# Kernel optimization log

Measured on AMD Instinct MI355X. Metric: run time of the kernel, lower is better.

## Reference

```python
import jax, jax.numpy as jnp
import numpy as np

EPS = 1e-08
K_N = 10
K_E = 10
F_DIM = 512
SCALE = F_DIM ** -0.5
N_NODES = 16384
N_EDGES = 2048


def layernorm(x, w, b):
    mu = x.mean(axis=-1, keepdims=True)
    var = x.var(axis=-1, keepdims=True)
    return (x - mu) * jax.lax.rsqrt(var + 1e-5) * w + b


def mask_attn(attn, k):
    # topk along last dim, scatter boolean mask, elementwise masking
    _, idx = jax.lax.top_k(attn, k)
    rows = jnp.arange(attn.shape[0])[:, None]
    mask = jnp.zeros(attn.shape, dtype=bool).at[rows, idx].set(True)
    return attn * mask


def setup_inputs() -> dict:
    key = jax.random.key(0)
    ks = jax.random.split(key, 12)
    d, h = F_DIM, 512  # hidden = max(f_dim, 128)
    w = 0.02  # weight init scale to keep softmax unsaturated
    return {
        'inputs': jax.random.normal(ks[0], (N_NODES, d), jnp.float32),
        'noise': jax.random.normal(ks[1], (N_EDGES, d), jnp.float32),
        'edges_mu': jax.random.normal(ks[2], (1, d), jnp.float32),
        'edges_logsigma': jnp.zeros((1, d), jnp.float32),
        'Wq': jax.random.normal(ks[3], (d, d), jnp.float32) * w,
        'bq': jnp.zeros((d,), jnp.float32),
        'Wk': jax.random.normal(ks[4], (d, d), jnp.float32) * w,
        'bk': jnp.zeros((d,), jnp.float32),
        'Wv': jax.random.normal(ks[5], (d, d), jnp.float32) * w,
        'bv': jnp.zeros((d,), jnp.float32),
        'W1': jax.random.normal(ks[6], (2 * d, h), jnp.float32) * w,
        'b1': jnp.zeros((h,), jnp.float32),
        'W2': jax.random.normal(ks[7], (h, d), jnp.float32) * w,
        'b2': jnp.zeros((d,), jnp.float32),
        'ln_in_w': jnp.ones((d,), jnp.float32),
        'ln_in_b': jnp.zeros((d,), jnp.float32),
        'ln_e_w': jnp.ones((d,), jnp.float32),
        'ln_e_b': jnp.zeros((d,), jnp.float32),
    }


def reference(inputs, noise, edges_mu, edges_logsigma, Wq, bq, Wk, bk, Wv, bv,
              W1, b1, W2, b2, ln_in_w, ln_in_b, ln_e_w, ln_e_b):
    relu = jax.nn.relu
    # slot init: mu + sigma * noise  -> [n_s, d]
    edges = edges_mu + jnp.exp(edges_logsigma) * noise
    x = layernorm(inputs, ln_in_w, ln_in_b)          # [n, d]
    k = relu(x @ Wk + bk)                            # [n, d]
    v = relu(x @ Wv + bv)                            # [n, d]
    # single iteration (iters=1)
    e = layernorm(edges, ln_e_w, ln_e_b)             # [n_s, d]
    q = relu(e @ Wq + bq)                            # [n_s, d]
    dots = (q @ k.T) * SCALE                         # [n_s, n]
    attn = jax.nn.softmax(dots, axis=1) + EPS
    attn = attn / attn.sum(axis=1, keepdims=True)
    attn = mask_attn(attn, K_N)
    updates = attn @ v                               # [n_s, d]
    e = jnp.concatenate([e, updates], axis=1)        # [n_s, 2d]
    e = relu(e @ W1 + b1) @ W2 + b2                  # mlp -> [n_s, d]
    q2 = x @ Wq + bq                                 # note: no activation here
    k2 = relu(e @ Wk + bk)                           # [n_s, d]
    dots2 = (q2 @ k2.T) * SCALE                      # [n, n_s]
    attn_v = jax.nn.softmax(dots2, axis=1)
    H = mask_attn(attn_v, K_E)
    return e, H, dots2
```

## Files before the change

kernel.cpp:

```cpp
#include <hip/hip_runtime.h>
#include <stdint.h>


#define NN 16384
#define NE 2048
#define TOPK 10

static const float SCALE_F = 0.04419417382415922f;
#define EPS_F 1e-8f

using bf16x8  = __attribute__((ext_vector_type(8))) __bf16;
using floatx4 = __attribute__((ext_vector_type(4))) float;

__device__ __forceinline__ unsigned f_as_u(float f) {
  union { float f; unsigned u; } v; v.f = f; return v.u;
}
__device__ __forceinline__ float u_as_f(unsigned u) {
  union { unsigned u; float f; } v; v.u = u; return v.f;
}
__device__ __forceinline__ unsigned short f2bf(float f) {
  unsigned u = f_as_u(f);
  unsigned r = u + 0x7fffu + ((u >> 16) & 1u);
  return (unsigned short)(r >> 16);
}
__device__ __forceinline__ float bf2f(unsigned short h) {
  return u_as_f(((unsigned)h) << 16);
}

__device__ __forceinline__ void glds16(const unsigned short* g, unsigned short* l) {
  __builtin_amdgcn_global_load_lds(
      (const __attribute__((address_space(1))) unsigned int*)g,
      (__attribute__((address_space(3))) unsigned int*)l, 16, 0, 0);
}

__device__ __forceinline__ unsigned fkey(float f) {
  unsigned u = f_as_u(f);
  return (u & 0x80000000u) ? ~u : (u | 0x80000000u);
}
__device__ __forceinline__ float funkey(unsigned k) {
  unsigned u = (k & 0x80000000u) ? (k ^ 0x80000000u) : ~k;
  return u_as_f(u);
}
__device__ __forceinline__ unsigned long long packkc(float v, int col) {
  return ((unsigned long long)fkey(v) << 32) | (unsigned)(~(unsigned)col);
}
__device__ __forceinline__ int unpack_col(unsigned long long w) {
  return (int)(~(unsigned)(w & 0xFFFFFFFFull));
}
__device__ __forceinline__ float unpack_val(unsigned long long w) {
  return funkey((unsigned)(w >> 32));
}
__device__ __forceinline__ unsigned long long shfl_xor_u64(unsigned long long x, int m) {
  unsigned lo = (unsigned)x, hi = (unsigned)(x >> 32);
  lo = __shfl_xor(lo, m, 64);
  hi = __shfl_xor(hi, m, 64);
  return ((unsigned long long)hi << 32) | lo;
}

__global__ void transpose_cast_kernel(const float* __restrict__ src,
                                      unsigned short* __restrict__ dhi,
                                      unsigned short* __restrict__ dlo,
                                      int K, int N) {
  __shared__ float tile[32][33];
  int n0 = blockIdx.x * 32, k0 = blockIdx.y * 32;
  int tx = threadIdx.x, ty = threadIdx.y;
  for (int r = ty; r < 32; r += 8)
    tile[r][tx] = src[(size_t)(k0 + r) * N + n0 + tx];
  __syncthreads();
  for (int r = ty; r < 32; r += 8) {
    float v = tile[tx][r];
    size_t o = (size_t)(n0 + r) * K + k0 + tx;
    unsigned short h = f2bf(v);
    dhi[o] = h;
    if (dlo) dlo[o] = f2bf(v - bf2f(h));
  }
}

__global__ void transpose_cast3_kernel(const float* __restrict__ s0,
                                       const float* __restrict__ s1,
                                       const float* __restrict__ s2,
                                       unsigned short* __restrict__ dhi) {
  __shared__ float tile[32][33];
  const float* src = blockIdx.z == 0 ? s0 : (blockIdx.z == 1 ? s1 : s2);
  unsigned short* d = dhi + (size_t)blockIdx.z * 512 * 512;
  int n0 = blockIdx.x * 32, k0 = blockIdx.y * 32;
  int tx = threadIdx.x, ty = threadIdx.y;
  for (int r = ty; r < 32; r += 8)
    tile[r][tx] = src[(size_t)(k0 + r) * 512 + n0 + tx];
  __syncthreads();
  for (int r = ty; r < 32; r += 8)
    d[(size_t)(n0 + r) * 512 + k0 + tx] = f2bf(tile[tx][r]);
}

__device__ __forceinline__ float block_sum_256(float v, float* sm4) {
#pragma unroll
  for (int off = 32; off; off >>= 1) v += __shfl_down(v, off, 64);
  __syncthreads();
  if ((threadIdx.x & 63) == 0) sm4[threadIdx.x >> 6] = v;
  __syncthreads();
  return (sm4[0] + sm4[1]) + (sm4[2] + sm4[3]);
}

__global__ __launch_bounds__(256) void ln_x_kernel(
    const float* __restrict__ in, const float* __restrict__ w,
    const float* __restrict__ b, unsigned short* __restrict__ out_hi) {
  __shared__ float sm4[4];
  int row = blockIdx.x, tid = threadIdx.x;
  const float* r = in + (size_t)row * 512;
  float x0 = r[tid], x1 = r[tid + 256];
  float mu = block_sum_256(x0 + x1, sm4) * (1.0f / 512.0f);
  float d0 = x0 - mu, d1 = x1 - mu;
  float var = block_sum_256(d0 * d0 + d1 * d1, sm4) * (1.0f / 512.0f);
  float rs = rsqrtf(var + 1e-5f);
  out_hi[(size_t)row * 512 + tid]       = f2bf(d0 * rs * w[tid] + b[tid]);
  out_hi[(size_t)row * 512 + tid + 256] = f2bf(d1 * rs * w[tid + 256] + b[tid + 256]);
}

__global__ __launch_bounds__(256) void ln_e_kernel(
    const float* __restrict__ noise, const float* __restrict__ mu_e,
    const float* __restrict__ ls_e, const float* __restrict__ w,
    const float* __restrict__ b, unsigned short* __restrict__ e1_hi,
    unsigned short* __restrict__ e1_lo) {
  __shared__ float sm4[4];
  int row = blockIdx.x, tid = threadIdx.x;
  const float* r = noise + (size_t)row * 512;
  float x0 = mu_e[tid] + expf(ls_e[tid]) * r[tid];
  float x1 = mu_e[tid + 256] + expf(ls_e[tid + 256]) * r[tid + 256];
  float mu = block_sum_256(x0 + x1, sm4) * (1.0f / 512.0f);
  float d0 = x0 - mu, d1 = x1 - mu;
  float var = block_sum_256(d0 * d0 + d1 * d1, sm4) * (1.0f / 512.0f);
  float rs = rsqrtf(var + 1e-5f);
  float y0 = d0 * rs * w[tid] + b[tid];
  float y1 = d1 * rs * w[tid + 256] + b[tid + 256];
  size_t o = (size_t)row * 1024;
  unsigned short h0 = f2bf(y0), h1 = f2bf(y1);
  e1_hi[o + tid] = h0;             e1_lo[o + tid] = f2bf(y0 - bf2f(h0));
  e1_hi[o + tid + 256] = h1;       e1_lo[o + tid + 256] = f2bf(y1 - bf2f(h1));
}

#define GEMM128_CORE(A_, B_, bm_, bn_, acc_, SMEM_)                            \
  unsigned short* As = (unsigned short*)(SMEM_);                               \
  unsigned short* Bs = (unsigned short*)(SMEM_) + 4096;                        \
  {                                                                            \
    const unsigned short* gA0 = (A_) + ((bm_) + (tid >> 2)) * 512 + ((tid & 3) << 3); \
    const unsigned short* gA1 = gA0 + 64 * 512;                                \
    const unsigned short* gB0 = (B_) + ((bn_) + (tid >> 2)) * 512 + ((tid & 3) << 3); \
    const unsigned short* gB1 = gB0 + 64 * 512;                                \
    unsigned short* dA0 = &As[wave * 512];                                     \
    unsigned short* dA1 = &As[2048 + wave * 512];                              \
    unsigned short* dB0 = &Bs[wave * 512];                                     \
    unsigned short* dB1 = &Bs[2048 + wave * 512];                              \
    for (int k0 = 0; k0 < 512; k0 += 32) {                                     \
      glds16(gA0 + k0, dA0);                                                   \
      glds16(gA1 + k0, dA1);                                                   \
      glds16(gB0 + k0, dB0);                                                   \
      glds16(gB1 + k0, dB1);                                                   \
      __syncthreads();                                                         \
      bf16x8 af0 = *(const bf16x8*)&As[(wave * 32 + lrow) * 32 + quad * 8];    \
      bf16x8 af1 = *(const bf16x8*)&As[(wave * 32 + 16 + lrow) * 32 + quad * 8]; \
      _Pragma("unroll")                                                        \
      for (int t = 0; t < 8; ++t) {                                            \
        bf16x8 bfr = *(const bf16x8*)&Bs[(t * 16 + lrow) * 32 + quad * 8];     \
        acc_[0][t] = __builtin_amdgcn_mfma_f32_16x16x32_bf16(af0, bfr, acc_[0][t], 0, 0, 0); \
        acc_[1][t] = __builtin_amdgcn_mfma_f32_16x16x32_bf16(af1, bfr, acc_[1][t], 0, 0, 0); \
      }                                                                        \
      __syncthreads();                                                         \
    }                                                                          \
  }

#define XCD_PANEL_MAP(mt_, nt_, owns_m_)                                       \
  int bid = (int)blockIdx.x, xcd = bid & 7, idx = bid >> 3;                    \
  int per = ((owns_m_) ? (mt_) : (nt_)) >> 3;                                  \
  int pa = idx % per, pb = idx / per;                                          \
  size_t bm = (size_t)((owns_m_) ? (xcd * per + pa) : pb) * 128;               \
  size_t bn = (size_t)((owns_m_) ? pb : (xcd * per + pa)) * 128;

__global__ __launch_bounds__(256) void gemm128_dots_kernel(
    const unsigned short* __restrict__ A, const unsigned short* __restrict__ B,
    float alpha, float* __restrict__ C, int ldc, int mt, int nt, int owns_m) {
  __shared__ __align__(16) char smem[33792];
  int tid = threadIdx.x, wave = tid >> 6, lane = tid & 63;
  int lrow = lane & 15, quad = lane >> 4;
  XCD_PANEL_MAP(mt, nt, owns_m)
  floatx4 zero4 = {0.f, 0.f, 0.f, 0.f};
  floatx4 acc[2][8];
#pragma unroll
  for (int i = 0; i < 2; ++i)
#pragma unroll
    for (int t = 0; t < 8; ++t) acc[i][t] = zero4;
  GEMM128_CORE(A, B, bm, bn, acc, smem)
  __syncthreads();
  float* wb = (float*)smem + wave * (16 * 132);
#pragma unroll
  for (int i = 0; i < 2; ++i) {
#pragma unroll
    for (int t = 0; t < 8; ++t)
#pragma unroll
      for (int r = 0; r < 4; ++r)
        wb[(quad * 4 + r) * 132 + t * 16 + lrow] = acc[i][t][r] * alpha;
    __syncthreads();
    size_t rowbase = bm + wave * 32 + i * 16;
#pragma unroll
    for (int p = 0; p < 8; ++p) {
      int rr = p * 2 + (lane >> 5);
      float4 v = *(const float4*)&wb[rr * 132 + ((lane & 31) << 2)];
      *(float4*)&C[(rowbase + rr) * (size_t)ldc + bn + ((lane & 31) << 2)] = v;
    }
    __syncthreads();
  }
}

__global__ __launch_bounds__(256) void gemm128_kvq_kernel(
    const unsigned short* __restrict__ A, const unsigned short* __restrict__ B,
    const float* __restrict__ bk, const float* __restrict__ bv,
    const float* __restrict__ bq,
    unsigned short* __restrict__ khi, unsigned short* __restrict__ vhi,
    unsigned short* __restrict__ q2hi) {
  __shared__ __align__(16) char smem[17408];
  int tid = threadIdx.x, wave = tid >> 6, lane = tid & 63;
  int lrow = lane & 15, quad = lane >> 4;
  XCD_PANEL_MAP(128, 12, 1)
  floatx4 zero4 = {0.f, 0.f, 0.f, 0.f};
  floatx4 acc[2][8];
#pragma unroll
  for (int i = 0; i < 2; ++i)
#pragma unroll
    for (int t = 0; t < 8; ++t) acc[i][t] = zero4;
  GEMM128_CORE(A, B, bm, bn, acc, smem)
  int mat = (int)(bn >> 9);
  int colbase = (int)(bn & 511);
  const float* bias = mat == 0 ? bk : (mat == 1 ? bv : bq);
  unsigned short* dst = mat == 0 ? khi : (mat == 1 ? vhi : q2hi);
  bool relu = mat < 2;
  __syncthreads();
  unsigned short* wb = (unsigned short*)smem + wave * (16 * 136);
#pragma unroll
  for (int i = 0; i < 2; ++i) {
#pragma unroll
    for (int t = 0; t < 8; ++t) {
      float bvv = bias[colbase + t * 16 + lrow];
#pragma unroll
      for (int r = 0; r < 4; ++r) {
        float v = acc[i][t][r] + bvv;
        if (relu) v = fmaxf(v, 0.0f);
        wb[(quad * 4 + r) * 136 + t * 16 + lrow] = f2bf(v);
      }
    }
    __syncthreads();
    size_t rowbase = bm + wave * 32 + i * 16;
#pragma unroll
    for (int p = 0; p < 4; ++p) {
      int rr = p * 4 + (lane >> 4);
      uint4 v = *(const uint4*)&wb[rr * 136 + ((lane & 15) << 3)];
      *(uint4*)&dst[(rowbase + rr) * 512 + colbase + ((lane & 15) << 3)] = v;
    }
    __syncthreads();
  }
}

template <bool SPLIT, bool RELU, bool HAS_BIAS, bool WF32, bool WHI, bool WLO>
__global__ __launch_bounds__(256) void gemm64_kernel(
    const unsigned short* __restrict__ Ahi, const unsigned short* __restrict__ Alo, int lda,
    const unsigned short* __restrict__ Bhi, const unsigned short* __restrict__ Blo, int K,
    const float* __restrict__ bias, float alpha,
    float* __restrict__ Cf, int ldc,
    unsigned short* __restrict__ Chi, unsigned short* __restrict__ Clo, int ldcb) {
  __shared__ __align__(16) unsigned short AsH[64 * 32];
  __shared__ __align__(16) unsigned short BsH[64 * 32];
  __shared__ __align__(16) unsigned short AsL[64 * 32];
  __shared__ __align__(16) unsigned short BsL[64 * 32];
  int tid = threadIdx.x, wave = tid >> 6, lane = tid & 63;
  int lrow = lane & 15, quad = lane >> 4;
  size_t bm = (size_t)blockIdx.x * 64, bn = (size_t)blockIdx.y * 64;
  int row = tid >> 2, off = (tid & 3) << 3;
  size_t aoff = (bm + row) * (size_t)lda + off;
  size_t boff = (bn + row) * (size_t)K + off;

  floatx4 zero4 = {0.f, 0.f, 0.f, 0.f};
  floatx4 acc[4];
#pragma unroll
  for (int t = 0; t < 4; ++t) acc[t] = zero4;

  for (int k0 = 0; k0 < K; k0 += 32) {
    uint4 ah = *(const uint4*)(Ahi + aoff + k0);
    uint4 bh = *(const uint4*)(Bhi + boff + k0);
    uint4 al, bl;
    if (SPLIT) {
      al = *(const uint4*)(Alo + aoff + k0);
      bl = *(const uint4*)(Blo + boff + k0);
    }
    __syncthreads();
    *(uint4*)&AsH[tid * 8] = ah;
    *(uint4*)&BsH[tid * 8] = bh;
    if (SPLIT) {
      *(uint4*)&AsL[tid * 8] = al;
      *(uint4*)&BsL[tid * 8] = bl;
    }
    __syncthreads();
    int ai = (wave * 16 + lrow) * 32 + quad * 8;
    bf16x8 aH = *(const bf16x8*)&AsH[ai];
    bf16x8 aL;
    if (SPLIT) aL = *(const bf16x8*)&AsL[ai];
#pragma unroll
    for (int t = 0; t < 4; ++t) {
      int bi = (t * 16 + lrow) * 32 + quad * 8;
      bf16x8 bH = *(const bf16x8*)&BsH[bi];
      acc[t] = __builtin_amdgcn_mfma_f32_16x16x32_bf16(aH, bH, acc[t], 0, 0, 0);
      if (SPLIT) {
        bf16x8 bL = *(const bf16x8*)&BsL[bi];
        acc[t] = __builtin_amdgcn_mfma_f32_16x16x32_bf16(aH, bL, acc[t], 0, 0, 0);
        acc[t] = __builtin_amdgcn_mfma_f32_16x16x32_bf16(aL, bH, acc[t], 0, 0, 0);
      }
    }
  }
  size_t row0 = bm + wave * 16 + quad * 4;
#pragma unroll
  for (int t = 0; t < 4; ++t) {
    int col = (int)bn + t * 16 + lrow;
    float bv = HAS_BIAS ? bias[col] : 0.0f;
#pragma unroll
    for (int r = 0; r < 4; ++r) {
      float v = acc[t][r] * alpha + bv;
      if (RELU) v = fmaxf(v, 0.0f);
      if (WF32) Cf[(row0 + r) * (size_t)ldc + col] = v;
      if (WHI) {
        unsigned short h = f2bf(v);
        Chi[(row0 + r) * (size_t)ldcb + col] = h;
        if (WLO) Clo[(row0 + r) * (size_t)ldcb + col] = f2bf(v - bf2f(h));
      }
    }
  }
}

#define INSERT4(lv, li, v, col)                                   \
  do {                                                            \
    if ((v) > lv[3]) {                                            \
      float cv_ = (v); int ci_ = (col);                           \
      _Pragma("unroll")                                           \
      for (int j_ = 0; j_ < 4; ++j_) {                            \
        bool sw_ = (cv_ > lv[j_]);                                \
        float tv_ = sw_ ? lv[j_] : cv_;                           \
        int ti_ = sw_ ? li[j_] : ci_;                              \
        lv[j_] = sw_ ? cv_ : lv[j_];                              \
        li[j_] = sw_ ? ci_ : li[j_];                              \
        cv_ = tv_; ci_ = ti_;                                     \
      }                                                           \
    }                                                             \
  } while (0)

__global__ __launch_bounds__(256) void attn1_kernel(
    const float* __restrict__ dots,
    const unsigned short* __restrict__ vhi,
    unsigned short* __restrict__ e1_hi, unsigned short* __restrict__ e1_lo) {
  __shared__ float sm_m[4], sm_s[4];
  __shared__ unsigned long long wbest[4];
  __shared__ unsigned long long wkey_s[TOPK];

  int tid = threadIdx.x, wave = tid >> 6, lane = tid & 63;
  int rowi = blockIdx.x;
  const float4* r4 = (const float4*)(dots + (size_t)rowi * NN);

  float lv[4]; int li[4];
#pragma unroll
  for (int j = 0; j < 4; ++j) { lv[j] = -INFINITY; li[j] = 0x7fffffff; }
  unsigned long long selmask = 0ull;
  int taken = 0;

  float m_loc = -INFINITY, s_loc = 0.0f;
  for (int i = 0; i < 16; ++i) {
    float4 q = r4[tid + (i << 8)];
#pragma unroll
    for (int c = 0; c < 4; ++c) {
      float v = (&q.x)[c];
      int col = ((tid + (i << 8)) << 2) + c;
      if (v > m_loc) {
        s_loc = s_loc * __expf(m_loc - v) + 1.0f;
        m_loc = v;
      } else {
        s_loc += __expf(v - m_loc);
      }
      INSERT4(lv, li, v, col);
    }
  }
#pragma unroll
  for (int sft = 32; sft; sft >>= 1) {
    float om = __shfl_xor(m_loc, sft, 64);
    float os = __shfl_xor(s_loc, sft, 64);
    float M = fmaxf(m_loc, om);
    s_loc = s_loc * __expf(m_loc - M) + os * __expf(om - M);
    m_loc = M;
  }
  if (lane == 0) { sm_m[wave] = m_loc; sm_s[wave] = s_loc; }
  __syncthreads();
  float M = fmaxf(fmaxf(sm_m[0], sm_m[1]), fmaxf(sm_m[2], sm_m[3]));
  float Z = sm_s[0] * __expf(sm_m[0] - M) + sm_s[1] * __expf(sm_m[1] - M) +
            sm_s[2] * __expf(sm_m[2] - M) + sm_s[3] * __expf(sm_m[3] - M);

  for (int rnd = 0; rnd < TOPK; ++rnd) {
    unsigned long long key;
    if (taken < 4) {
      key = packkc(lv[0], li[0]);
    } else {
      key = 0ull;
      for (int i = 0; i < 16; ++i) {
        float4 q = r4[tid + (i << 8)];
#pragma unroll
        for (int c = 0; c < 4; ++c) {
          int sl = i * 4 + c;
          if (!((selmask >> sl) & 1ull)) {
            int col = ((tid + (i << 8)) << 2) + c;
            unsigned long long kk = packkc((&q.x)[c], col);
            if (kk > key) key = kk;
          }
        }
      }
    }
#pragma unroll
    for (int sft = 32; sft; sft >>= 1) {
      unsigned long long ok = shfl_xor_u64(key, sft);
      if (ok > key) key = ok;
    }
    if (lane == 0) wbest[wave] = key;
    __syncthreads();
    unsigned long long w = wbest[0];
    if (wbest[1] > w) w = wbest[1];
    if (wbest[2] > w) w = wbest[2];
    if (wbest[3] > w) w = wbest[3];
    if (tid == 0) wkey_s[rnd] = w;
    int wcol = unpack_col(w);
    if (((wcol >> 2) & 255) == tid) {
      int sl = ((wcol >> 10) << 2) | (wcol & 3);
      selmask |= (1ull << sl);
      if (taken < 4) {
#pragma unroll
        for (int j = 0; j < 3; ++j) { lv[j] = lv[j + 1]; li[j] = li[j + 1]; }
      }
      ++taken;
    }
    __syncthreads();
  }

  const float inv_den = 1.0f / (1.0f + (float)NN * EPS_F);
  float invZ = 1.0f / Z;
  float u0 = 0.f, u1 = 0.f;
#pragma unroll
  for (int j = 0; j < TOPK; ++j) {
    unsigned long long w = wkey_s[j];
    int col = unpack_col(w);
    float val = unpack_val(w);
    float a = (__expf(val - M) * invZ + EPS_F) * inv_den;
    const unsigned short* vr = vhi + (size_t)col * 512;
    u0 += a * bf2f(vr[tid]);
    u1 += a * bf2f(vr[tid + 256]);
  }
  size_t o = (size_t)rowi * 1024 + 512;
  unsigned short h0 = f2bf(u0), h1 = f2bf(u1);
  e1_hi[o + tid] = h0;             e1_lo[o + tid] = f2bf(u0 - bf2f(h0));
  e1_hi[o + tid + 256] = h1;       e1_lo[o + tid + 256] = f2bf(u1 - bf2f(h1));
}

__global__ __launch_bounds__(256) void attn2_kernel(const float* __restrict__ dots2,
                                                    float* __restrict__ Hout) {
  int tid = threadIdx.x, wave = tid >> 6, lane = tid & 63;
  int rowi = blockIdx.x * 4 + wave;
  const float4* r4 = (const float4*)(dots2 + (size_t)rowi * NE);

  float d[32];
  float m = -INFINITY;
#pragma unroll
  for (int i = 0; i < 8; ++i) {
    float4 q = r4[lane + (i << 6)];
#pragma unroll
    for (int c = 0; c < 4; ++c) {
      d[i * 4 + c] = (&q.x)[c];
      m = fmaxf(m, d[i * 4 + c]);
    }
  }
#pragma unroll
  for (int sft = 32; sft; sft >>= 1) m = fmaxf(m, __shfl_xor(m, sft, 64));

  float s = 0.f;
#pragma unroll
  for (int j = 0; j < 32; ++j) { d[j] = __expf(d[j] - m); s += d[j]; }
#pragma unroll
  for (int sft = 32; sft; sft >>= 1) s += __shfl_xor(s, sft, 64);
  float invZ = 1.0f / s;

  float lv[4]; int li[4];
#pragma unroll
  for (int j = 0; j < 4; ++j) { lv[j] = -INFINITY; li[j] = 0x7fffffff; }
#pragma unroll
  for (int i = 0; i < 8; ++i) {
#pragma unroll
    for (int c = 0; c < 4; ++c) {
      int col = ((lane + (i << 6)) << 2) + c;
      INSERT4(lv, li, d[i * 4 + c], col);
    }
  }

  unsigned selmask = 0;
  int taken = 0;
  for (int rnd = 0; rnd < TOPK; ++rnd) {
    unsigned long long key;
    if (taken < 4) {
      key = packkc(lv[0], li[0]);
    } else {
      key = 0ull;
#pragma unroll
      for (int j = 0; j < 32; ++j) {
        if (!((selmask >> j) & 1u)) {
          int col = ((lane + ((j >> 2) << 6)) << 2) + (j & 3);
          unsigned long long kk = packkc(d[j], col);
          if (kk > key) key = kk;
        }
      }
    }
#pragma unroll
    for (int sft = 32; sft; sft >>= 1) {
      unsigned long long ok = shfl_xor_u64(key, sft);
      if (ok > key) key = ok;
    }
    int wcol = unpack_col(key);
    if (((wcol >> 2) & 63) == lane) {
      int sl = ((wcol >> 8) << 2) | (wcol & 3);
      selmask |= (1u << sl);
      if (taken < 4) {
#pragma unroll
        for (int j = 0; j < 3; ++j) { lv[j] = lv[j + 1]; li[j] = li[j + 1]; }
      }
      ++taken;
    }
  }

  float* hr = Hout + (size_t)rowi * NE;
#pragma unroll
  for (int i = 0; i < 8; ++i) {
    float4 o;
#pragma unroll
    for (int c = 0; c < 4; ++c) {
      int sl = i * 4 + c;
      (&o.x)[c] = ((selmask >> sl) & 1u) ? d[sl] * invZ : 0.0f;
    }
    ((float4*)hr)[lane + (i << 6)] = o;
  }
}

extern "C" void kernel_launch(void* const* d_in, const int* in_sizes, int n_in,
                              void* d_out, int out_size, void* d_ws, size_t ws_size,
                              hipStream_t stream) {
  (void)in_sizes; (void)n_in; (void)out_size; (void)ws_size;
  const float* inputs  = (const float*)d_in[0];
  const float* noise   = (const float*)d_in[1];
  const float* edges_mu = (const float*)d_in[2];
  const float* edges_ls = (const float*)d_in[3];
  const float* Wq = (const float*)d_in[4];
  const float* bq = (const float*)d_in[5];
  const float* Wk = (const float*)d_in[6];
  const float* bk = (const float*)d_in[7];
  const float* Wv = (const float*)d_in[8];
  const float* bv = (const float*)d_in[9];
  const float* W1 = (const float*)d_in[10];
  const float* b1 = (const float*)d_in[11];
  const float* W2 = (const float*)d_in[12];
  const float* b2 = (const float*)d_in[13];
  const float* ln_in_w = (const float*)d_in[14];
  const float* ln_in_b = (const float*)d_in[15];
  const float* ln_e_w = (const float*)d_in[16];
  const float* ln_e_b = (const float*)d_in[17];

  float* out_e  = (float*)d_out;
  float* out_H  = out_e + (size_t)NE * 512;
  float* out_d2 = out_H + (size_t)NN * NE;

  const size_t MB = 1024 * 1024;
  unsigned char* hb = (unsigned char*)out_H;
  unsigned short* x_hi  = (unsigned short*)(hb);
  unsigned short* k_hi  = (unsigned short*)(hb + 16 * MB);
  unsigned short* v_hi  = (unsigned short*)(hb + 32 * MB);
  unsigned short* q2_hi = (unsigned short*)(hb + 48 * MB);
  unsigned short* WcatT = (unsigned short*)(hb + 64 * MB);
  unsigned short* W1Th  = (unsigned short*)(hb + 66 * MB);
  unsigned short* W1Tl  = (unsigned short*)(hb + 67 * MB);
  unsigned short* W2Th  = (unsigned short*)(hb + 68 * MB);
  unsigned short* W2Tl  = (unsigned short*)(hb + 68 * MB + 512 * 1024);
  unsigned short* e1_hi = (unsigned short*)(hb + 70 * MB);
  unsigned short* e1_lo = (unsigned short*)(hb + 74 * MB);
  unsigned short* q_hi  = (unsigned short*)(hb + 78 * MB);
  unsigned short* h_hi  = (unsigned short*)(hb + 80 * MB);
  unsigned short* h_lo  = (unsigned short*)(hb + 82 * MB);
  unsigned short* e_hi  = (unsigned short*)(hb + 84 * MB);
  unsigned short* WkT   = WcatT;
  unsigned short* WqT   = WcatT + (size_t)1024 * 512;
  float* dots = out_d2;
  unsigned short* k2_hi = (unsigned short*)d_ws;

  dim3 tb(256);
  dim3 t32(32, 8);

  transpose_cast3_kernel<<<dim3(16, 16, 3), t32, 0, stream>>>(Wk, Wv, Wq, WcatT);
  transpose_cast_kernel<<<dim3(16, 32), t32, 0, stream>>>(W1, W1Th, W1Tl, 1024, 512);
  transpose_cast_kernel<<<dim3(16, 16), t32, 0, stream>>>(W2, W2Th, W2Tl, 512, 512);

  ln_x_kernel<<<NN, tb, 0, stream>>>(inputs, ln_in_w, ln_in_b, x_hi);
  ln_e_kernel<<<NE, tb, 0, stream>>>(noise, edges_mu, edges_ls, ln_e_w, ln_e_b, e1_hi, e1_lo);

  gemm128_kvq_kernel<<<dim3(1536), tb, 0, stream>>>(
      x_hi, WcatT, bk, bv, bq, k_hi, v_hi, q2_hi);
  gemm64_kernel<false, true, true, false, true, false><<<dim3(32, 8), tb, 0, stream>>>(
      e1_hi, nullptr, 1024, WqT, nullptr, 512, bq, 1.f, nullptr, 0, q_hi, nullptr, 512);
  gemm128_dots_kernel<<<dim3(2048), tb, 0, stream>>>(
      q_hi, k_hi, SCALE_F, dots, NN, 16, 128, 0);
  attn1_kernel<<<NE, tb, 0, stream>>>(dots, v_hi, e1_hi, e1_lo);
  gemm64_kernel<true, true, true, false, true, true><<<dim3(32, 8), tb, 0, stream>>>(
      e1_hi, e1_lo, 1024, W1Th, W1Tl, 1024, b1, 1.f, nullptr, 0, h_hi, h_lo, 512);
  gemm64_kernel<true, false, true, true, true, false><<<dim3(32, 8), tb, 0, stream>>>(
      h_hi, h_lo, 512, W2Th, W2Tl, 512, b2, 1.f, out_e, 512, e_hi, nullptr, 512);
  gemm64_kernel<false, true, true, false, true, false><<<dim3(32, 8), tb, 0, stream>>>(
      e_hi, nullptr, 512, WkT, nullptr, 512, bk, 1.f, nullptr, 0, k2_hi, nullptr, 512);
  gemm128_dots_kernel<<<dim3(2048), tb, 0, stream>>>(
      q2_hi, k2_hi, SCALE_F, out_d2, NE, 128, 16, 1);
  attn2_kernel<<<NN / 4, tb, 0, stream>>>(out_d2, out_H);
}
```

Baseline: 571.3 us.

## Merge prep kernels, fold q GEMM into kvq, widen GEMM K-tile with swizzled LDS

Three weight-transpose launches become one kernel, and the two layernorm launches become one, which cuts launch count. The separate q projection GEMM is folded into the kvq GEMM launch as 64 extra blocks. The 128x128 GEMM core now loads a 64-wide K slice per iteration into an XOR-swizzled shared-memory layout, halving the number of barrier pairs and aiming to reduce LDS bank conflicts. The gemm64 kernel also register-prefetches the next K slice, at the cost of larger shared-memory use and more registers.

```diff
diff --git a/kernel.cpp b/kernel.cpp
--- a/kernel.cpp
+++ b/kernel.cpp
@@ -57,15 +57,33 @@
   return ((unsigned long long)hi << 32) | lo;
 }
 
-__global__ void transpose_cast_kernel(const float* __restrict__ src,
-                                      unsigned short* __restrict__ dhi,
-                                      unsigned short* __restrict__ dlo,
-                                      int K, int N) {
+__global__ void transpose_all_kernel(
+    const float* __restrict__ Wk, const float* __restrict__ Wv,
+    const float* __restrict__ Wq, unsigned short* __restrict__ WcatT,
+    const float* __restrict__ W1, unsigned short* __restrict__ W1Th,
+    unsigned short* __restrict__ W1Tl,
+    const float* __restrict__ W2, unsigned short* __restrict__ W2Th,
+    unsigned short* __restrict__ W2Tl) {
   __shared__ float tile[32][33];
+  int z = blockIdx.z;
+  if (z != 3 && blockIdx.y >= 16) return;
+  const float* src;
+  unsigned short* dhi;
+  unsigned short* dlo;
+  int K;
+  if (z < 3) {
+    src = z == 0 ? Wk : (z == 1 ? Wv : Wq);
+    dhi = WcatT + (size_t)z * 512 * 512;
+    dlo = nullptr; K = 512;
+  } else if (z == 3) {
+    src = W1; dhi = W1Th; dlo = W1Tl; K = 1024;
+  } else {
+    src = W2; dhi = W2Th; dlo = W2Tl; K = 512;
+  }
   int n0 = blockIdx.x * 32, k0 = blockIdx.y * 32;
   int tx = threadIdx.x, ty = threadIdx.y;
   for (int r = ty; r < 32; r += 8)
-    tile[r][tx] = src[(size_t)(k0 + r) * N + n0 + tx];
+    tile[r][tx] = src[(size_t)(k0 + r) * 512 + n0 + tx];
   __syncthreads();
   for (int r = ty; r < 32; r += 8) {
     float v = tile[tx][r];
@@ -76,22 +94,6 @@
   }
 }
 
-__global__ void transpose_cast3_kernel(const float* __restrict__ s0,
-                                       const float* __restrict__ s1,
-                                       const float* __restrict__ s2,
-                                       unsigned short* __restrict__ dhi) {
-  __shared__ float tile[32][33];
-  const float* src = blockIdx.z == 0 ? s0 : (blockIdx.z == 1 ? s1 : s2);
-  unsigned short* d = dhi + (size_t)blockIdx.z * 512 * 512;
-  int n0 = blockIdx.x * 32, k0 = blockIdx.y * 32;
-  int tx = threadIdx.x, ty = threadIdx.y;
-  for (int r = ty; r < 32; r += 8)
-    tile[r][tx] = src[(size_t)(k0 + r) * 512 + n0 + tx];
-  __syncthreads();
-  for (int r = ty; r < 32; r += 8)
-    d[(size_t)(n0 + r) * 512 + k0 + tx] = f2bf(tile[tx][r]);
-}
-
 __device__ __forceinline__ float block_sum_256(float v, float* sm4) {
 #pragma unroll
   for (int off = 32; off; off >>= 1) v += __shfl_down(v, off, 64);
@@ -101,79 +103,90 @@
   return (sm4[0] + sm4[1]) + (sm4[2] + sm4[3]);
 }
 
-__global__ __launch_bounds__(256) void ln_x_kernel(
+__global__ __launch_bounds__(256) void ln_all_kernel(
     const float* __restrict__ in, const float* __restrict__ w,
-    const float* __restrict__ b, unsigned short* __restrict__ out_hi) {
-  __shared__ float sm4[4];
-  int row = blockIdx.x, tid = threadIdx.x;
-  const float* r = in + (size_t)row * 512;
-  float x0 = r[tid], x1 = r[tid + 256];
-  float mu = block_sum_256(x0 + x1, sm4) * (1.0f / 512.0f);
-  float d0 = x0 - mu, d1 = x1 - mu;
-  float var = block_sum_256(d0 * d0 + d1 * d1, sm4) * (1.0f / 512.0f);
-  float rs = rsqrtf(var + 1e-5f);
-  out_hi[(size_t)row * 512 + tid]       = f2bf(d0 * rs * w[tid] + b[tid]);
-  out_hi[(size_t)row * 512 + tid + 256] = f2bf(d1 * rs * w[tid + 256] + b[tid + 256]);
-}
-
-__global__ __launch_bounds__(256) void ln_e_kernel(
+    const float* __restrict__ b, unsigned short* __restrict__ out_hi,
     const float* __restrict__ noise, const float* __restrict__ mu_e,
-    const float* __restrict__ ls_e, const float* __restrict__ w,
-    const float* __restrict__ b, unsigned short* __restrict__ e1_hi,
+    const float* __restrict__ ls_e, const float* __restrict__ we,
+    const float* __restrict__ be, unsigned short* __restrict__ e1_hi,
     unsigned short* __restrict__ e1_lo) {
   __shared__ float sm4[4];
   int row = blockIdx.x, tid = threadIdx.x;
-  const float* r = noise + (size_t)row * 512;
-  float x0 = mu_e[tid] + expf(ls_e[tid]) * r[tid];
-  float x1 = mu_e[tid + 256] + expf(ls_e[tid + 256]) * r[tid + 256];
-  float mu = block_sum_256(x0 + x1, sm4) * (1.0f / 512.0f);
-  float d0 = x0 - mu, d1 = x1 - mu;
-  float var = block_sum_256(d0 * d0 + d1 * d1, sm4) * (1.0f / 512.0f);
-  float rs = rsqrtf(var + 1e-5f);
-  float y0 = d0 * rs * w[tid] + b[tid];
-  float y1 = d1 * rs * w[tid + 256] + b[tid + 256];
-  size_t o = (size_t)row * 1024;
-  unsigned short h0 = f2bf(y0), h1 = f2bf(y1);
-  e1_hi[o + tid] = h0;             e1_lo[o + tid] = f2bf(y0 - bf2f(h0));
-  e1_hi[o + tid + 256] = h1;       e1_lo[o + tid + 256] = f2bf(y1 - bf2f(h1));
-}
-
-#define GEMM128_CORE(A_, B_, bm_, bn_, acc_, SMEM_)                            \
+  if (row < NN) {
+    const float* r = in + (size_t)row * 512;
+    float x0 = r[tid], x1 = r[tid + 256];
+    float mu = block_sum_256(x0 + x1, sm4) * (1.0f / 512.0f);
+    float d0 = x0 - mu, d1 = x1 - mu;
+    float var = block_sum_256(d0 * d0 + d1 * d1, sm4) * (1.0f / 512.0f);
+    float rs = rsqrtf(var + 1e-5f);
+    out_hi[(size_t)row * 512 + tid]       = f2bf(d0 * rs * w[tid] + b[tid]);
+    out_hi[(size_t)row * 512 + tid + 256] = f2bf(d1 * rs * w[tid + 256] + b[tid + 256]);
+  } else {
+    row -= NN;
+    const float* r = noise + (size_t)row * 512;
+    float x0 = mu_e[tid] + expf(ls_e[tid]) * r[tid];
+    float x1 = mu_e[tid + 256] + expf(ls_e[tid + 256]) * r[tid + 256];
+    float mu = block_sum_256(x0 + x1, sm4) * (1.0f / 512.0f);
+    float d0 = x0 - mu, d1 = x1 - mu;
+    float var = block_sum_256(d0 * d0 + d1 * d1, sm4) * (1.0f / 512.0f);
+    float rs = rsqrtf(var + 1e-5f);
+    float y0 = d0 * rs * we[tid] + be[tid];
+    float y1 = d1 * rs * we[tid + 256] + be[tid + 256];
+    size_t o = (size_t)row * 1024;
+    unsigned short h0 = f2bf(y0), h1 = f2bf(y1);
+    e1_hi[o + tid] = h0;             e1_lo[o + tid] = f2bf(y0 - bf2f(h0));
+    e1_hi[o + tid + 256] = h1;       e1_lo[o + tid + 256] = f2bf(y1 - bf2f(h1));
+  }
+}
+
+#define GEMM128_CORE(A_, LDA_, B_, bm_, bn_, acc_, SMEM_)                      \
   unsigned short* As = (unsigned short*)(SMEM_);                               \
-  unsigned short* Bs = (unsigned short*)(SMEM_) + 4096;                        \
+  unsigned short* Bs = (unsigned short*)(SMEM_) + 8192;                        \
   {                                                                            \
-    const unsigned short* gA0 = (A_) + ((bm_) + (tid >> 2)) * 512 + ((tid & 3) << 3); \
-    const unsigned short* gA1 = gA0 + 64 * 512;                                \
-    const unsigned short* gB0 = (B_) + ((bn_) + (tid >> 2)) * 512 + ((tid & 3) << 3); \
-    const unsigned short* gB1 = gB0 + 64 * 512;                                \
-    unsigned short* dA0 = &As[wave * 512];                                     \
-    unsigned short* dA1 = &As[2048 + wave * 512];                              \
-    unsigned short* dB0 = &Bs[wave * 512];                                     \
-    unsigned short* dB1 = &Bs[2048 + wave * 512];                              \
-    for (int k0 = 0; k0 < 512; k0 += 32) {                                     \
-      glds16(gA0 + k0, dA0);                                                   \
-      glds16(gA1 + k0, dA1);                                                   \
-      glds16(gB0 + k0, dB0);                                                   \
-      glds16(gB1 + k0, dB1);                                                   \
+    int srow = tid >> 3;                                                       \
+    int scol = ((tid ^ (tid >> 3)) & 7) << 3;                                  \
+    const unsigned short* gA = (A_) + ((bm_) + srow) * (size_t)(LDA_) + scol;  \
+    const unsigned short* gB = (B_) + ((bn_) + srow) * (size_t)512 + scol;     \
+    unsigned short* dA = As + wave * 512;                                      \
+    unsigned short* dB = Bs + wave * 512;                                      \
+    int swz0 = (quad ^ (lrow & 7)) << 3;                                       \
+    int swz1 = swz0 ^ 32;                                                      \
+    int aoff0 = (wave * 32 + lrow) * 64;                                       \
+    int aoff1 = aoff0 + 16 * 64;                                               \
+    int boffl = lrow * 64;                                                     \
+    for (int k0 = 0; k0 < 512; k0 += 64) {                                     \
+      glds16(gA + k0, dA);                                                     \
+      glds16(gA + 32 * (size_t)(LDA_) + k0, dA + 2048);                        \
+      glds16(gA + 64 * (size_t)(LDA_) + k0, dA + 4096);                        \
+      glds16(gA + 96 * (size_t)(LDA_) + k0, dA + 6144);                        \
+      glds16(gB + k0, dB);                                                     \
+      glds16(gB + 32 * 512 + k0, dB + 2048);                                   \
+      glds16(gB + 64 * 512 + k0, dB + 4096);                                   \
+      glds16(gB + 96 * 512 + k0, dB + 6144);                                   \
       __syncthreads();                                                         \
-      bf16x8 af0 = *(const bf16x8*)&As[(wave * 32 + lrow) * 32 + quad * 8];    \
-      bf16x8 af1 = *(const bf16x8*)&As[(wave * 32 + 16 + lrow) * 32 + quad * 8]; \
+      bf16x8 af00 = *(const bf16x8*)&As[aoff0 + swz0];                         \
+      bf16x8 af01 = *(const bf16x8*)&As[aoff0 + swz1];                         \
+      bf16x8 af10 = *(const bf16x8*)&As[aoff1 + swz0];                         \
+      bf16x8 af11 = *(const bf16x8*)&As[aoff1 + swz1];                         \
       _Pragma("unroll")                                                        \
       for (int t = 0; t < 8; ++t) {                                            \
-        bf16x8 bfr = *(const bf16x8*)&Bs[(t * 16 + lrow) * 32 + quad * 8];     \
-        acc_[0][t] = __builtin_amdgcn_mfma_f32_16x16x32_bf16(af0, bfr, acc_[0][t], 0, 0, 0); \
-        acc_[1][t] = __builtin_amdgcn_mfma_f32_16x16x32_bf16(af1, bfr, acc_[1][t], 0, 0, 0); \
+        bf16x8 bf0 = *(const bf16x8*)&Bs[t * 1024 + boffl + swz0];             \
+        bf16x8 bf1 = *(const bf16x8*)&Bs[t * 1024 + boffl + swz1];             \
+        acc_[0][t] = __builtin_amdgcn_mfma_f32_16x16x32_bf16(af00, bf0, acc_[0][t], 0, 0, 0); \
+        acc_[0][t] = __builtin_amdgcn_mfma_f32_16x16x32_bf16(af01, bf1, acc_[0][t], 0, 0, 0); \
+        acc_[1][t] = __builtin_amdgcn_mfma_f32_16x16x32_bf16(af10, bf0, acc_[1][t], 0, 0, 0); \
+        acc_[1][t] = __builtin_amdgcn_mfma_f32_16x16x32_bf16(af11, bf1, acc_[1][t], 0, 0, 0); \
       }                                                                        \
       __syncthreads();                                                         \
     }                                                                          \
   }
 
 #define XCD_PANEL_MAP(mt_, nt_, owns_m_)                                       \
-  int bid = (int)blockIdx.x, xcd = bid & 7, idx = bid >> 3;                    \
+  int xcd = bid & 7, idx = bid >> 3;                                           \
   int per = ((owns_m_) ? (mt_) : (nt_)) >> 3;                                  \
   int pa = idx % per, pb = idx / per;                                          \
-  size_t bm = (size_t)((owns_m_) ? (xcd * per + pa) : pb) * 128;               \
-  size_t bn = (size_t)((owns_m_) ? pb : (xcd * per + pa)) * 128;
+  bm = (size_t)((owns_m_) ? (xcd * per + pa) : pb) * 128;                      \
+  bn = (size_t)((owns_m_) ? pb : (xcd * per + pa)) * 128;
 
 __global__ __launch_bounds__(256) void gemm128_dots_kernel(
     const unsigned short* __restrict__ A, const unsigned short* __restrict__ B,
@@ -181,6 +194,8 @@
   __shared__ __align__(16) char smem[33792];
   int tid = threadIdx.x, wave = tid >> 6, lane = tid & 63;
   int lrow = lane & 15, quad = lane >> 4;
+  int bid = (int)blockIdx.x;
+  size_t bm, bn;
   XCD_PANEL_MAP(mt, nt, owns_m)
   floatx4 zero4 = {0.f, 0.f, 0.f, 0.f};
   floatx4 acc[2][8];
@@ -188,7 +203,7 @@
   for (int i = 0; i < 2; ++i)
 #pragma unroll
     for (int t = 0; t < 8; ++t) acc[i][t] = zero4;
-  GEMM128_CORE(A, B, bm, bn, acc, smem)
+  GEMM128_CORE(A, 512, B, bm, bn, acc, smem)
   __syncthreads();
   float* wb = (float*)smem + wave * (16 * 132);
 #pragma unroll
@@ -211,27 +226,44 @@
 }
 
 __global__ __launch_bounds__(256) void gemm128_kvq_kernel(
-    const unsigned short* __restrict__ A, const unsigned short* __restrict__ B,
+    const unsigned short* __restrict__ X, const unsigned short* __restrict__ E1,
+    const unsigned short* __restrict__ B,
     const float* __restrict__ bk, const float* __restrict__ bv,
     const float* __restrict__ bq,
     unsigned short* __restrict__ khi, unsigned short* __restrict__ vhi,
-    unsigned short* __restrict__ q2hi) {
-  __shared__ __align__(16) char smem[17408];
+    unsigned short* __restrict__ q2hi, unsigned short* __restrict__ qhi) {
+  __shared__ __align__(16) char smem[32768];
   int tid = threadIdx.x, wave = tid >> 6, lane = tid & 63;
   int lrow = lane & 15, quad = lane >> 4;
-  XCD_PANEL_MAP(128, 12, 1)
+  int bid = (int)blockIdx.x;
+  size_t bm, bn;
+  const unsigned short* Aptr;
+  int lda;
+  unsigned short* dst;
+  const float* bias;
+  bool relu;
+  if (bid < 1536) {
+    XCD_PANEL_MAP(128, 12, 1)
+    Aptr = X; lda = 512;
+    int mat = (int)(bn >> 9);
+    bias = mat == 0 ? bk : (mat == 1 ? bv : bq);
+    dst = mat == 0 ? khi : (mat == 1 ? vhi : q2hi);
+    relu = mat < 2;
+  } else {
+    int qb = bid - 1536;
+    bm = (size_t)(qb >> 2) * 128;
+    bn = 1024 + (size_t)(qb & 3) * 128;
+    Aptr = E1; lda = 1024;
+    dst = qhi; bias = bq; relu = true;
+  }
+  int colbase = (int)(bn & 511);
   floatx4 zero4 = {0.f, 0.f, 0.f, 0.f};
   floatx4 acc[2][8];
 #pragma unroll
   for (int i = 0; i < 2; ++i)
 #pragma unroll
     for (int t = 0; t < 8; ++t) acc[i][t] = zero4;
-  GEMM128_CORE(A, B, bm, bn, acc, smem)
-  int mat = (int)(bn >> 9);
-  int colbase = (int)(bn & 511);
-  const float* bias = mat == 0 ? bk : (mat == 1 ? bv : bq);
-  unsigned short* dst = mat == 0 ? khi : (mat == 1 ? vhi : q2hi);
-  bool relu = mat < 2;
+  GEMM128_CORE(Aptr, lda, B, bm, bn, acc, smem)
   __syncthreads();
   unsigned short* wb = (unsigned short*)smem + wave * (16 * 136);
 #pragma unroll
@@ -281,14 +313,14 @@
 #pragma unroll
   for (int t = 0; t < 4; ++t) acc[t] = zero4;
 
+  uint4 ah = *(const uint4*)(Ahi + aoff);
+  uint4 bh = *(const uint4*)(Bhi + boff);
+  uint4 al, bl;
+  if (SPLIT) {
+    al = *(const uint4*)(Alo + aoff);
+    bl = *(const uint4*)(Blo + boff);
+  }
   for (int k0 = 0; k0 < K; k0 += 32) {
-    uint4 ah = *(const uint4*)(Ahi + aoff + k0);
-    uint4 bh = *(const uint4*)(Bhi + boff + k0);
-    uint4 al, bl;
-    if (SPLIT) {
-      al = *(const uint4*)(Alo + aoff + k0);
-      bl = *(const uint4*)(Blo + boff + k0);
-    }
     __syncthreads();
     *(uint4*)&AsH[tid * 8] = ah;
     *(uint4*)&BsH[tid * 8] = bh;
@@ -297,6 +329,14 @@
       *(uint4*)&BsL[tid * 8] = bl;
     }
     __syncthreads();
+    if (k0 + 32 < K) {
+      ah = *(const uint4*)(Ahi + aoff + k0 + 32);
+      bh = *(const uint4*)(Bhi + boff + k0 + 32);
+      if (SPLIT) {
+        al = *(const uint4*)(Alo + aoff + k0 + 32);
+        bl = *(const uint4*)(Blo + boff + k0 + 32);
+      }
+    }
     int ai = (wave * 16 + lrow) * 32 + quad * 8;
     bf16x8 aH = *(const bf16x8*)&AsH[ai];
     bf16x8 aL;
@@ -590,24 +630,20 @@
   unsigned short* h_lo  = (unsigned short*)(hb + 82 * MB);
   unsigned short* e_hi  = (unsigned short*)(hb + 84 * MB);
   unsigned short* WkT   = WcatT;
-  unsigned short* WqT   = WcatT + (size_t)1024 * 512;
   float* dots = out_d2;
   unsigned short* k2_hi = (unsigned short*)d_ws;
 
   dim3 tb(256);
   dim3 t32(32, 8);
 
-  transpose_cast3_kernel<<<dim3(16, 16, 3), t32, 0, stream>>>(Wk, Wv, Wq, WcatT);
-  transpose_cast_kernel<<<dim3(16, 32), t32, 0, stream>>>(W1, W1Th, W1Tl, 1024, 512);
-  transpose_cast_kernel<<<dim3(16, 16), t32, 0, stream>>>(W2, W2Th, W2Tl, 512, 512);
-
-  ln_x_kernel<<<NN, tb, 0, stream>>>(inputs, ln_in_w, ln_in_b, x_hi);
-  ln_e_kernel<<<NE, tb, 0, stream>>>(noise, edges_mu, edges_ls, ln_e_w, ln_e_b, e1_hi, e1_lo);
-
-  gemm128_kvq_kernel<<<dim3(1536), tb, 0, stream>>>(
-      x_hi, WcatT, bk, bv, bq, k_hi, v_hi, q2_hi);
-  gemm64_kernel<false, true, true, false, true, false><<<dim3(32, 8), tb, 0, stream>>>(
-      e1_hi, nullptr, 1024, WqT, nullptr, 512, bq, 1.f, nullptr, 0, q_hi, nullptr, 512);
+  transpose_all_kernel<<<dim3(16, 32, 5), t32, 0, stream>>>(
+      Wk, Wv, Wq, WcatT, W1, W1Th, W1Tl, W2, W2Th, W2Tl);
+  ln_all_kernel<<<NN + NE, tb, 0, stream>>>(
+      inputs, ln_in_w, ln_in_b, x_hi,
+      noise, edges_mu, edges_ls, ln_e_w, ln_e_b, e1_hi, e1_lo);
+
+  gemm128_kvq_kernel<<<dim3(1600), tb, 0, stream>>>(
+      x_hi, e1_hi, WcatT, bk, bv, bq, k_hi, v_hi, q2_hi, q_hi);
   gemm128_dots_kernel<<<dim3(2048), tb, 0, stream>>>(
       q_hi, k_hi, SCALE_F, dots, NN, 16, 128, 0);
   attn1_kernel<<<NE, tb, 0, stream>>>(dots, v_hi, e1_hi, e1_lo);
```

Result: faster. 547.2 us (-4.2%).
